# Optimization experiments

Hardware: AMD Instinct MI355X
Metric: run time of the kernel (lower is better)

The kernel has to match this reference:

```python
import jax, jax.numpy as jnp
import numpy as np

B, S, E, H = 2, 2048, 1024, 16
D = E // H  # head_dim = 64


def setup_inputs() -> dict:
    key = jax.random.key(0)
    ks = jax.random.split(key, 12)
    s = 1.0 / np.sqrt(E)
    return {
        "queries": jax.random.normal(ks[0], (B, S, E), jnp.float32),
        "keys": jax.random.normal(ks[1], (B, S, E), jnp.float32),
        "values": jax.random.normal(ks[2], (B, S, E), jnp.float32),
        "mask": jnp.zeros((B, 1, S, S), jnp.float32),
        "Wq": jax.random.normal(ks[3], (E, E), jnp.float32) * s,
        "bq": jnp.zeros((E,), jnp.float32),
        "Wk": jax.random.normal(ks[4], (E, E), jnp.float32) * s,
        "bk": jnp.zeros((E,), jnp.float32),
        "Wv": jax.random.normal(ks[5], (E, E), jnp.float32) * s,
        "bv": jnp.zeros((E,), jnp.float32),
        "Wo": jax.random.normal(ks[6], (E, E), jnp.float32) * s,
        "bo": jnp.zeros((E,), jnp.float32),
    }


def reference(queries, keys, values, mask, Wq, bq, Wk, bk, Wv, bv, Wo, bo):
    # QKV projections, then split heads: [B,S,E] -> [B,H,S,D]
    def split_heads(x):
        return x.reshape(B, S, H, D).transpose(0, 2, 1, 3)

    Q = split_heads(queries @ Wq + bq)
    K = split_heads(keys @ Wk + bk)
    V = split_heads(values @ Wv + bv)
    scale = jnp.sqrt(jnp.asarray(D, jnp.float32))
    # [B,H,S,S] attention scores
    scores = jnp.einsum("bhqd,bhkd->bhqk", Q, K) / scale
    scores = scores + mask * -10000.0
    weights = jax.nn.softmax(scores, axis=-1)
    # [B,H,S,D] -> [B,S,E]
    out = jnp.einsum("bhqk,bhkd->bhqd", weights, V)
    out = out.transpose(0, 2, 1, 3).reshape(B, S, E)
    return out @ Wo + bo
```

## Files before the change

kernel.cpp:

```cpp
#include <hip/hip_runtime.h>
#include <hip/hip_bf16.h>
#include <stdint.h>

#define B_ 2
#define S_ 2048
#define E_ 1024
#define H_ 16
#define D_ 64
#define LOG2E 1.4426950408889634f

typedef unsigned short ubf;
typedef __attribute__((ext_vector_type(8))) short bh8;
typedef __attribute__((ext_vector_type(4))) float fx4;
typedef __attribute__((ext_vector_type(16))) float fx16;

__device__ __forceinline__ ubf f2bf(float f) {
  unsigned u = __float_as_uint(f);
  unsigned r = (u + 0x7fffu + ((u >> 16) & 1u)) >> 16;
  return (ubf)r;
}

__device__ __forceinline__ unsigned cvtpk(float lo, float hi2) {
  unsigned r;
  asm("v_cvt_pk_bf16_f32 %0, %1, %2" : "=v"(r) : "v"(lo), "v"(hi2));
  return r;
}

__device__ __forceinline__ void pl32swap(unsigned& a, unsigned& b) {
  asm("v_permlane32_swap_b32 %0, %1" : "+v"(a), "+v"(b));
}

__device__ __forceinline__ void gl_lds16(const void* g, void* l) {
  __builtin_amdgcn_global_load_lds(
      (const __attribute__((address_space(1))) void*)g,
      (__attribute__((address_space(3))) void*)l, 16, 0, 0);
}

__global__ void prep(const float* __restrict__ q, const float* __restrict__ k,
                     const float* __restrict__ v, const float* __restrict__ mask,
                     ubf* __restrict__ dst0, int* __restrict__ flagarr) {
  const int z = blockIdx.z;
  const int tid = threadIdx.x;
  const int stride = gridDim.x * blockDim.x;
  if (z == 3) {
    int any = 0;
    const int n4m = (B_ * S_ * S_) / 4;
    for (int j = blockIdx.x * blockDim.x + tid; j < n4m; j += stride) {
      float4 x = ((const float4*)mask)[j];
      any |= (x.x != 0.f) | (x.y != 0.f) | (x.z != 0.f) | (x.w != 0.f);
    }
    int wany = __any(any != 0) ? 1 : 0;
    if ((tid & 63) == 0) flagarr[blockIdx.x * 4 + (tid >> 6)] = wany;
    return;
  }
  const float* src = (z == 0) ? q : (z == 1) ? k : v;
  ubf* dst = dst0 + (size_t)z * (B_ * S_ * E_);
  const int n4 = (B_ * S_ * E_) / 4;
  for (int j = blockIdx.x * blockDim.x + tid; j < n4; j += stride) {
    float4 x = ((const float4*)src)[j];
    ushort4 o;
    o.x = f2bf(x.x); o.y = f2bf(x.y); o.z = f2bf(x.z); o.w = f2bf(x.w);
    ((ushort4*)dst)[j] = o;
  }
}

__global__ void wtrans4(const float* __restrict__ Wq, const float* __restrict__ Wk,
                        const float* __restrict__ Wv, const float* __restrict__ Wo,
                        ubf* __restrict__ Wt0) {
  __shared__ float t[32][33];
  int z = blockIdx.z;
  const float* W = (z == 0) ? Wq : (z == 1) ? Wk : (z == 2) ? Wv : Wo;
  ubf* Wt = Wt0 + (size_t)z * (E_ * E_);
  int kb = blockIdx.x, nb = blockIdx.y;
  int c = threadIdx.x & 31, r0 = threadIdx.x >> 5;
#pragma unroll
  for (int rr = 0; rr < 32; rr += 8)
    t[r0 + rr][c] = W[(size_t)(kb * 32 + r0 + rr) * E_ + nb * 32 + c];
  __syncthreads();
#pragma unroll
  for (int rr = 0; rr < 32; rr += 8)
    Wt[(size_t)(nb * 32 + r0 + rr) * E_ + kb * 32 + c] = f2bf(t[c][r0 + rr]);
}

__global__ void __launch_bounds__(256, 6)
gemm_qkv(const ubf* __restrict__ X, const ubf* __restrict__ Wt,
         const float* __restrict__ bq, const float* __restrict__ bk,
         const float* __restrict__ bv, ubf* __restrict__ Out) {
  constexpr int K = 1024;
  __shared__ ubf Asm[2][128 * 32];
  __shared__ ubf Bsm[2][64 * 32];
  const int z = blockIdx.z;
  const ubf* A  = (z == 2) ? (Wt + 2u * 1048576u) : (X + (size_t)z * 4194304u);
  const ubf* Bt = (z == 2) ? (X + 2u * 4194304u) : (Wt + (size_t)z * 1048576u);
  const float* bias = (z == 0) ? bq : (z == 1) ? bk : bv;
  ubf* Cout = Out + (size_t)z * 4194304u;

  const int bx0 = blockIdx.x;
  const int swz = (bx0 & 7) * 64 + (bx0 >> 3);
  int bm, bn;
  if (z == 2) {
    bm = (swz >> 3) & 7;
    bn = ((swz >> 6) << 3) | (swz & 7);
  } else {
    bm = swz >> 4;
    bn = swz & 15;
  }

  const int tid = threadIdx.x;
  const int lane = tid & 63, w = tid >> 6;
  const int wm = w >> 1, wn = w & 1;
  const int g = lane >> 4, c15 = lane & 15;

  const fx4 FZ = {0.f, 0.f, 0.f, 0.f};
  fx4 acc[4][2];
#pragma unroll
  for (int m = 0; m < 4; m++)
#pragma unroll
    for (int n = 0; n < 2; n++) acc[m][n] = FZ;

  auto stage = [&](int buf, int k0) {
#pragma unroll
    for (int i = 0; i < 2; i++) {
      int s = i * 256 + tid;
      int row = s >> 2, cc = s & 3;
      int sc = cc ^ ((row >> 1) & 3);
      gl_lds16(A + (size_t)(bm * 128 + row) * K + k0 + sc * 8,
               (char*)&Asm[buf][0] + (i * 256 + (tid & 192)) * 16);
    }
    {
      int row = tid >> 2, cc = tid & 3;
      int sc = cc ^ ((row >> 1) & 3);
      gl_lds16(Bt + (size_t)(bn * 64 + row) * K + k0 + sc * 8,
               (char*)&Bsm[buf][0] + (tid & 192) * 16);
    }
  };

  stage(0, 0);
  for (int t = 0; t < K / 32; t++) {
    int cur = t & 1;
    if (t + 1 < K / 32) {
      stage(cur ^ 1, (t + 1) * 32);
      asm volatile("s_waitcnt vmcnt(3)" ::: "memory");
    } else {
      asm volatile("s_waitcnt vmcnt(0)" ::: "memory");
    }
    __builtin_amdgcn_s_barrier();
    bh8 a[4], b[2];
#pragma unroll
    for (int m = 0; m < 4; m++) {
      int row = wm * 64 + m * 16 + c15;
      int ch = g ^ ((row >> 1) & 3);
      a[m] = *(const bh8*)((const char*)&Asm[cur][0] + row * 64 + ch * 16);
    }
#pragma unroll
    for (int n = 0; n < 2; n++) {
      int row = wn * 32 + n * 16 + c15;
      int ch = g ^ ((row >> 1) & 3);
      b[n] = *(const bh8*)((const char*)&Bsm[cur][0] + row * 64 + ch * 16);
    }
    __builtin_amdgcn_s_setprio(1);
#pragma unroll
    for (int m = 0; m < 4; m++)
#pragma unroll
      for (int n = 0; n < 2; n++)
        acc[m][n] = __builtin_amdgcn_mfma_f32_16x16x32_bf16(a[m], b[n], acc[m][n], 0, 0, 0);
    __builtin_amdgcn_s_setprio(0);
    __builtin_amdgcn_s_barrier();
  }

#pragma unroll
  for (int m = 0; m < 4; m++) {
    int rbase = bm * 128 + wm * 64 + m * 16 + g * 4;
#pragma unroll
    for (int n = 0; n < 2; n++) {
      int col = bn * 64 + wn * 32 + n * 16 + c15;
#pragma unroll
      for (int r = 0; r < 4; r++) {
        int mrow = rbase + r;
        float val = acc[m][n][r];
        if (z <= 1) {
          val = val + bias[col];
          if (z == 0) val *= 0.125f * LOG2E;
          int bb = mrow >> 11, ss = mrow & 2047, hh = col >> 6, dd = col & 63;
          Cout[((size_t)(bb * H_ + hh) * S_ + ss) * D_ + dd] = f2bf(val);
        } else {
          val = val + bias[mrow];
          int bb = col >> 11, ss = col & 2047, hh = mrow >> 6, dd = mrow & 63;
          Cout[((size_t)(bb * H_ + hh) * D_ + dd) * S_ + ss] = f2bf(val);
        }
      }
    }
  }
}

__global__ void __launch_bounds__(256, 4)
gemm_out(const ubf* __restrict__ A, const ubf* __restrict__ Bt,
         const float* __restrict__ bias, float* __restrict__ Cout, int N) {
  constexpr int K = 1024;
  __shared__ ubf Asm[2][64 * 32];
  __shared__ ubf Bsm[2][64 * 32];
  const int tid = threadIdx.x;
  const int lane = tid & 63, w = tid >> 6;
  const int wm = w >> 1, wn = w & 1;
  const int bid = blockIdx.x;
  const int swz = (bid & 7) * 128 + (bid >> 3);
  const int bm = swz >> 4, bn = swz & 15;
  const int g = lane >> 4, c15 = lane & 15;

  const fx4 FZ = {0.f, 0.f, 0.f, 0.f};
  fx4 acc[2][2];
#pragma unroll
  for (int m = 0; m < 2; m++)
#pragma unroll
    for (int n = 0; n < 2; n++) acc[m][n] = FZ;

  auto stage = [&](int buf, int k0) {
    int row = tid >> 2, cc = tid & 3;
    int sc = cc ^ ((row >> 1) & 3);
    gl_lds16(A + (size_t)(bm * 64 + row) * K + k0 + sc * 8,
             (char*)&Asm[buf][0] + (tid & 192) * 16);
    gl_lds16(Bt + (size_t)(bn * 64 + row) * K + k0 + sc * 8,
             (char*)&Bsm[buf][0] + (tid & 192) * 16);
  };

  stage(0, 0);
  for (int t = 0; t < K / 32; t++) {
    int cur = t & 1;
    if (t + 1 < K / 32) {
      stage(cur ^ 1, (t + 1) * 32);
      asm volatile("s_waitcnt vmcnt(2)" ::: "memory");
    } else {
      asm volatile("s_waitcnt vmcnt(0)" ::: "memory");
    }
    __builtin_amdgcn_s_barrier();
    bh8 a[2], b[2];
#pragma unroll
    for (int m = 0; m < 2; m++) {
      int row = wm * 32 + m * 16 + c15;
      int ch = g ^ ((row >> 1) & 3);
      a[m] = *(const bh8*)((const char*)&Asm[cur][0] + row * 64 + ch * 16);
    }
#pragma unroll
    for (int n = 0; n < 2; n++) {
      int row = wn * 32 + n * 16 + c15;
      int ch = g ^ ((row >> 1) & 3);
      b[n] = *(const bh8*)((const char*)&Bsm[cur][0] + row * 64 + ch * 16);
    }
    __builtin_amdgcn_s_setprio(1);
#pragma unroll
    for (int m = 0; m < 2; m++)
#pragma unroll
      for (int n = 0; n < 2; n++)
        acc[m][n] = __builtin_amdgcn_mfma_f32_16x16x32_bf16(a[m], b[n], acc[m][n], 0, 0, 0);
    __builtin_amdgcn_s_setprio(0);
    __builtin_amdgcn_s_barrier();
  }

#pragma unroll
  for (int m = 0; m < 2; m++) {
    int rbase = bm * 64 + wm * 32 + m * 16 + g * 4;
#pragma unroll
    for (int n = 0; n < 2; n++) {
      int col = bn * 64 + wn * 32 + n * 16 + c15;
#pragma unroll
      for (int r = 0; r < 4; r++)
        Cout[(size_t)(rbase + r) * N + col] = acc[m][n][r] + bias[col];
    }
  }
}

#define ROWQ(r) (((r) & 3) + 8 * ((r) >> 2) + 4 * hi)

__global__ void __launch_bounds__(512, 2)
flash_fast(const ubf* __restrict__ Q, const ubf* __restrict__ Kh,
           const ubf* __restrict__ Vt, ubf* __restrict__ AO) {
  __shared__ char lds[65536];
  const int tid = threadIdx.x, lane = tid & 63, w = tid >> 6;
  const int grp = w >> 2, wq = w & 3, tin = tid & 255;
  const int l31 = lane & 31, hi = lane >> 5;
  const int bh = blockIdx.x;
  const int qb = blockIdx.y;
  const int b = bh >> 4, h = bh & 15;
  const int k00 = grp * (S_ / 2);
  constexpr int NT = (S_ / 2) / 64;

  const ubf* Qrow = Q + ((size_t)bh * S_ + qb * 128 + wq * 32 + l31) * D_;
  bh8 q4[4];
#pragma unroll
  for (int kf = 0; kf < 4; kf++) q4[kf] = *(const bh8*)(Qrow + kf * 16 + hi * 8);

  fx16 acc0, acc1, ZF;
#pragma unroll
  for (int i = 0; i < 16; i++) { acc0[i] = 0.f; acc1[i] = 0.f; ZF[i] = 0.f; }
  float2 lr2 = make_float2(0.f, 0.f);

  const ubf* Kg = Kh + (size_t)bh * S_ * D_;
  const ubf* Vg = Vt + (size_t)bh * D_ * S_;
  char* Kbase = lds + grp * 32768;

  auto stage = [&](int buf, int k0) {
    char* Kb = Kbase + buf * 16384;
#pragma unroll
    for (int i = 0; i < 2; i++) {
      int s = i * 256 + tin;
      int row = s >> 3, cc = s & 7;
      int sw = cc ^ (row & 7);
      gl_lds16(Kg + (size_t)(k0 + row) * D_ + sw * 8,
               Kb + (i * 256 + (tin & 192)) * 16);
      gl_lds16(Vg + (size_t)row * S_ + k0 + sw * 8,
               Kb + 8192 + (i * 256 + (tin & 192)) * 16);
    }
  };

  stage(0, k00);

  for (int t = 0; t < NT; t++) {
    int cur = t & 1;
    if (t + 1 < NT) {
      stage(cur ^ 1, k00 + (t + 1) * 64);
      asm volatile("s_waitcnt vmcnt(4)" ::: "memory");
    } else {
      asm volatile("s_waitcnt vmcnt(0)" ::: "memory");
    }
    __builtin_amdgcn_s_barrier();
    const char* Kc = Kbase + cur * 16384;
    const char* Vc = Kc + 8192;

#pragma unroll
    for (int h2 = 0; h2 < 2; h2++) {
      fx16 sc;
      __builtin_amdgcn_s_setprio(1);
      {
        int ch = hi ^ (l31 & 7);
        bh8 ak = *(const bh8*)(Kc + (h2 * 32 + l31) * 128 + ch * 16);
        sc = __builtin_amdgcn_mfma_f32_32x32x16_bf16(ak, q4[0], ZF, 0, 0, 0);
      }
#pragma unroll
      for (int kf = 1; kf < 4; kf++) {
        int ch = (2 * kf + hi) ^ (l31 & 7);
        bh8 ak = *(const bh8*)(Kc + (h2 * 32 + l31) * 128 + ch * 16);
        sc = __builtin_amdgcn_mfma_f32_32x32x16_bf16(ak, q4[kf], sc, 0, 0, 0);
      }
      __builtin_amdgcn_s_setprio(0);

#pragma unroll
      for (int i = 0; i < 8; i++) {
        float p0 = __builtin_amdgcn_exp2f(sc[2 * i]);
        float p1 = __builtin_amdgcn_exp2f(sc[2 * i + 1]);
        sc[2 * i] = p0; sc[2 * i + 1] = p1;
        lr2.x += p0; lr2.y += p1;
      }

      unsigned pk[8];
#pragma unroll
      for (int i = 0; i < 8; i++) pk[i] = cvtpk(sc[2 * i], sc[2 * i + 1]);
      pl32swap(pk[0], pk[2]); pl32swap(pk[1], pk[3]);
      pl32swap(pk[4], pk[6]); pl32swap(pk[5], pk[7]);

      __builtin_amdgcn_s_setprio(1);
#pragma unroll
      for (int kk = 0; kk < 2; kk++) {
        int KF = 2 * h2 + kk;
        int ch = (2 * KF + hi) ^ (l31 & 7);
        bh8 bv0 = *(const bh8*)(Vc + l31 * 128 + ch * 16);
        bh8 bv1 = *(const bh8*)(Vc + (32 + l31) * 128 + ch * 16);
        unsigned wa[4] = {pk[4 * kk], pk[4 * kk + 1], pk[4 * kk + 2], pk[4 * kk + 3]};
        bh8 pa = *(bh8*)wa;
        acc0 = __builtin_amdgcn_mfma_f32_32x32x16_bf16(pa, bv0, acc0, 0, 0, 0);
        acc1 = __builtin_amdgcn_mfma_f32_32x32x16_bf16(pa, bv1, acc1, 0, 0, 0);
      }
      __builtin_amdgcn_s_setprio(0);
    }
    __builtin_amdgcn_s_barrier();
  }

  float lrun = lr2.x + lr2.y;
  float lsum = lrun + __shfl_xor(lrun, 32);
  float* shacc = (float*)lds;
  float* shml  = (float*)(lds + 34816);
  if (grp == 1) {
    float* p = shacc + (size_t)(wq * 64 + lane) * 34;
#pragma unroll
    for (int r = 0; r < 16; r++) { p[r] = acc0[r]; p[16 + r] = acc1[r]; }
    if (hi == 0) shml[wq * 32 + l31] = lsum;
  }
  __syncthreads();
  if (grp == 0) {
    const float* p = shacc + (size_t)(wq * 64 + lane) * 34;
#pragma unroll
    for (int r = 0; r < 16; r++) {
      int q2 = ROWQ(r);
      float l0 = __shfl(lsum, q2);
      float inv = 1.0f / (l0 + shml[wq * 32 + q2]);
      size_t base = ((size_t)(b * S_ + qb * 128 + wq * 32 + q2)) * E_ + h * 64;
      AO[base + l31] = f2bf((acc0[r] + p[r]) * inv);
      AO[base + 32 + l31] = f2bf((acc1[r] + p[16 + r]) * inv);
    }
  }
}

#define PV_STEP(KF, W0, W1, W2, W3)                                             \
    {                                                                           \
      unsigned wa[4] = {W0, W1, W2, W3};                                        \
      bh8 pa = *(bh8*)wa;                                                       \
      int ch = (2 * (KF) + hi) ^ (l31 & 7);                                     \
      bh8 bv0 = *(const bh8*)(Vc + l31 * 128 + ch * 16);                        \
      acc0 = __builtin_amdgcn_mfma_f32_32x32x16_bf16(pa, bv0, acc0, 0, 0, 0);   \
      bh8 bv1 = *(const bh8*)(Vc + (32 + l31) * 128 + ch * 16);                 \
      acc1 = __builtin_amdgcn_mfma_f32_32x32x16_bf16(pa, bv1, acc1, 0, 0, 0);   \
    }

__global__ void __launch_bounds__(256, 4)
flash_masked(const ubf* __restrict__ Q, const ubf* __restrict__ Kh,
             const ubf* __restrict__ Vt, const float* __restrict__ mask,
             const int* __restrict__ flagarr, ubf* __restrict__ AO) {
  __shared__ int anyf;
  if (threadIdx.x == 0) anyf = 0;
  __syncthreads();
  {
    int a = 0;
#pragma unroll
    for (int i = 0; i < 8; i++) a |= flagarr[threadIdx.x + i * 256];
    if (a) anyf = 1;
  }
  __syncthreads();
  if (anyf == 0) return;

  __shared__ ubf Ksm[2][64 * 64];
  __shared__ ubf Vsm[2][64 * 64];
  const int tid = threadIdx.x, lane = tid & 63, w = tid >> 6;
  const int l31 = lane & 31, hi = lane >> 5;
  const int bh = blockIdx.x;
  const int qb = blockIdx.y;
  const int b = bh >> 4, h = bh & 15;
  const int qg = qb * 128 + w * 32 + l31;
  constexpr int NT = S_ / 64;

  const ubf* Qrow = Q + ((size_t)bh * S_ + qg) * D_;
  bh8 q4[4];
#pragma unroll
  for (int kf = 0; kf < 4; kf++) q4[kf] = *(const bh8*)(Qrow + kf * 16 + hi * 8);

  fx16 acc0, acc1;
#pragma unroll
  for (int i = 0; i < 16; i++) { acc0[i] = 0.f; acc1[i] = 0.f; }
  float mrun = -3.0e38f, lrun = 0.f;

  const ubf* Kg = Kh + (size_t)bh * S_ * D_;
  const ubf* Vg = Vt + (size_t)bh * D_ * S_;

  auto stage = [&](int buf, int k0) {
#pragma unroll
    for (int i = 0; i < 2; i++) {
      int s = i * 256 + tid;
      int row = s >> 3, cc = s & 7;
      int sw = cc ^ (row & 7);
      gl_lds16(Kg + (size_t)(k0 + row) * D_ + sw * 8,
               (char*)&Ksm[buf][0] + (i * 256 + (tid & 192)) * 16);
      gl_lds16(Vg + (size_t)row * S_ + k0 + sw * 8,
               (char*)&Vsm[buf][0] + (i * 256 + (tid & 192)) * 16);
    }
  };

  stage(0, 0);
  __syncthreads();

  for (int t = 0; t < NT; t++) {
    int cur = t & 1;
    if (t + 1 < NT) stage(cur ^ 1, (t + 1) * 64);
    const char* Kc = (const char*)&Ksm[cur][0];
    const char* Vc = (const char*)&Vsm[cur][0];

#pragma unroll
    for (int h2 = 0; h2 < 2; h2++) {
      fx16 sc;
#pragma unroll
      for (int i = 0; i < 16; i++) sc[i] = 0.f;
#pragma unroll
      for (int kf = 0; kf < 4; kf++) {
        int ch = (2 * kf + hi) ^ (l31 & 7);
        bh8 ak = *(const bh8*)(Kc + (h2 * 32 + l31) * 128 + ch * 16);
        sc = __builtin_amdgcn_mfma_f32_32x32x16_bf16(ak, q4[kf], sc, 0, 0, 0);
      }
      const float* mq = mask + ((size_t)(b * S_ + qg)) * S_ + t * 64 + h2 * 32;
#pragma unroll
      for (int r = 0; r < 16; r++)
        sc[r] += mq[ROWQ(r)] * (-14426.950408889634f);

      float pm = sc[0];
#pragma unroll
      for (int r = 1; r < 16; r++) pm = fmaxf(pm, sc[r]);
      pm = fmaxf(pm, __shfl_xor(pm, 32));
      if (__any(pm - mrun > 11.5415603f)) {
        float mnew = fmaxf(mrun, pm);
        float al = exp2f(mrun - mnew);
        lrun *= al;
#pragma unroll
        for (int r = 0; r < 16; r++) {
          float alr = __shfl(al, ROWQ(r));
          acc0[r] *= alr;
          acc1[r] *= alr;
        }
        mrun = mnew;
      }
      float rsv[4] = {0.f, 0.f, 0.f, 0.f};
#pragma unroll
      for (int i = 0; i < 16; i++) {
        float p = exp2f(sc[i] - mrun);
        sc[i] = p;
        rsv[i & 3] += p;
      }
      lrun += (rsv[0] + rsv[1]) + (rsv[2] + rsv[3]);

      unsigned pk[8];
#pragma unroll
      for (int i = 0; i < 8; i++) pk[i] = cvtpk(sc[2 * i], sc[2 * i + 1]);
      pl32swap(pk[0], pk[2]); pl32swap(pk[1], pk[3]);
      pl32swap(pk[4], pk[6]); pl32swap(pk[5], pk[7]);

      PV_STEP(2 * h2,     pk[0], pk[1], pk[2], pk[3])
      PV_STEP(2 * h2 + 1, pk[4], pk[5], pk[6], pk[7])
    }
    __syncthreads();
  }

  float ltot = lrun + __shfl_xor(lrun, 32);
#pragma unroll
  for (int r = 0; r < 16; r++) {
    int q2 = ROWQ(r);
    float linv = 1.0f / __shfl(ltot, q2);
    size_t base = ((size_t)(b * S_ + qb * 128 + w * 32 + q2)) * E_ + h * 64;
    AO[base + l31] = f2bf(acc0[r] * linv);
    AO[base + 32 + l31] = f2bf(acc1[r] * linv);
  }
}

extern "C" void kernel_launch(void* const* d_in, const int* in_sizes, int n_in,
                              void* d_out, int out_size, void* d_ws, size_t ws_size,
                              hipStream_t stream) {
  (void)in_sizes; (void)n_in; (void)out_size; (void)ws_size;
  const float* q  = (const float*)d_in[0];
  const float* k  = (const float*)d_in[1];
  const float* v  = (const float*)d_in[2];
  const float* mask = (const float*)d_in[3];
  const float* Wq = (const float*)d_in[4];
  const float* bq = (const float*)d_in[5];
  const float* Wk = (const float*)d_in[6];
  const float* bk = (const float*)d_in[7];
  const float* Wv = (const float*)d_in[8];
  const float* bv = (const float*)d_in[9];
  const float* Wo = (const float*)d_in[10];
  const float* bo = (const float*)d_in[11];

  char* ws = (char*)d_ws;
  ubf* X    = (ubf*)(ws);
  ubf* Wt0  = (ubf*)(ws + 25165824);
  ubf* Qh   = (ubf*)(ws + 33554432);
  ubf* Kh   = (ubf*)(ws + 41943040);
  ubf* Vt   = (ubf*)(ws + 50331648);
  ubf* AO   = (ubf*)(ws + 58720256);
  int* flagarr = (int*)(ws + 67108864);

  ubf* Wot = Wt0 + 3145728;

  prep<<<dim3(512, 1, 4), 256, 0, stream>>>(q, k, v, mask, X, flagarr);
  wtrans4<<<dim3(32, 32, 4), 256, 0, stream>>>(Wq, Wk, Wv, Wo, Wt0);

  gemm_qkv<<<dim3(512, 1, 3), 256, 0, stream>>>(X, Wt0, bq, bk, bv, Qh);

  flash_fast<<<dim3(32, 16), 512, 0, stream>>>(Qh, Kh, Vt, AO);
  flash_masked<<<dim3(32, 16), 256, 0, stream>>>(Qh, Kh, Vt, mask, flagarr, AO);

  gemm_out<<<dim3(1024), 256, 0, stream>>>(AO, Wot, bo, (float*)d_out, 1024);
}
```

Measured before the change: 134.2 us.

## Fuse fp32-to-bf16 activation conversion into QKV projection GEMM loads

The prep kernel no longer converts q/k/v to a bf16 workspace. Instead, the QKV GEMM loads fp32 activations into registers, converts them with packed bf16 conversion, and writes them to swizzled LDS, while weights still go through direct global-to-LDS loads. This removes a full write and re-read of 24 MB of bf16 activations and one pass of the prep kernel. In exchange the GEMM reads fp32 data (twice the bytes per tile, and each tile is re-read across the N blocks), adds register pressure, and drops the occupancy hint from launch bounds. The new pipeline also waits on vmcnt(0) each iteration, which weakens load/compute overlap.

```diff
diff --git a/kernel.cpp b/kernel.cpp
--- a/kernel.cpp
+++ b/kernel.cpp
@@ -36,32 +36,17 @@
       (__attribute__((address_space(3))) void*)l, 16, 0, 0);
 }
 
-__global__ void prep(const float* __restrict__ q, const float* __restrict__ k,
-                     const float* __restrict__ v, const float* __restrict__ mask,
-                     ubf* __restrict__ dst0, int* __restrict__ flagarr) {
-  const int z = blockIdx.z;
+__global__ void maskscan(const float* __restrict__ mask, int* __restrict__ flagarr) {
   const int tid = threadIdx.x;
   const int stride = gridDim.x * blockDim.x;
-  if (z == 3) {
-    int any = 0;
-    const int n4m = (B_ * S_ * S_) / 4;
-    for (int j = blockIdx.x * blockDim.x + tid; j < n4m; j += stride) {
-      float4 x = ((const float4*)mask)[j];
-      any |= (x.x != 0.f) | (x.y != 0.f) | (x.z != 0.f) | (x.w != 0.f);
-    }
-    int wany = __any(any != 0) ? 1 : 0;
-    if ((tid & 63) == 0) flagarr[blockIdx.x * 4 + (tid >> 6)] = wany;
-    return;
-  }
-  const float* src = (z == 0) ? q : (z == 1) ? k : v;
-  ubf* dst = dst0 + (size_t)z * (B_ * S_ * E_);
-  const int n4 = (B_ * S_ * E_) / 4;
-  for (int j = blockIdx.x * blockDim.x + tid; j < n4; j += stride) {
-    float4 x = ((const float4*)src)[j];
-    ushort4 o;
-    o.x = f2bf(x.x); o.y = f2bf(x.y); o.z = f2bf(x.z); o.w = f2bf(x.w);
-    ((ushort4*)dst)[j] = o;
-  }
+  int any = 0;
+  const int n4m = (B_ * S_ * S_) / 4;
+  for (int j = blockIdx.x * blockDim.x + tid; j < n4m; j += stride) {
+    float4 x = ((const float4*)mask)[j];
+    any |= (x.x != 0.f) | (x.y != 0.f) | (x.z != 0.f) | (x.w != 0.f);
+  }
+  int wany = __any(any != 0) ? 1 : 0;
+  if ((tid & 63) == 0) flagarr[blockIdx.x * 4 + (tid >> 6)] = wany;
 }
 
 __global__ void wtrans4(const float* __restrict__ Wq, const float* __restrict__ Wk,
@@ -82,16 +67,18 @@
     Wt[(size_t)(nb * 32 + r0 + rr) * E_ + kb * 32 + c] = f2bf(t[c][r0 + rr]);
 }
 
-__global__ void __launch_bounds__(256, 6)
-gemm_qkv(const ubf* __restrict__ X, const ubf* __restrict__ Wt,
+__global__ void __launch_bounds__(256)
+gemm_qkv(const float* __restrict__ q, const float* __restrict__ k,
+         const float* __restrict__ v, const ubf* __restrict__ Wt,
          const float* __restrict__ bq, const float* __restrict__ bk,
          const float* __restrict__ bv, ubf* __restrict__ Out) {
   constexpr int K = 1024;
+  constexpr int NTT = K / 32;
   __shared__ ubf Asm[2][128 * 32];
   __shared__ ubf Bsm[2][64 * 32];
   const int z = blockIdx.z;
-  const ubf* A  = (z == 2) ? (Wt + 2u * 1048576u) : (X + (size_t)z * 4194304u);
-  const ubf* Bt = (z == 2) ? (X + 2u * 4194304u) : (Wt + (size_t)z * 1048576u);
+  const float* Fsrc = (z == 0) ? q : (z == 1) ? k : v;
+  const ubf* Wsrc = (z == 2) ? (Wt + 2u * 1048576u) : (Wt + (size_t)z * 1048576u);
   const float* bias = (z == 0) ? bq : (z == 1) ? bk : bv;
   ubf* Cout = Out + (size_t)z * 4194304u;
 
@@ -110,6 +97,7 @@
   const int lane = tid & 63, w = tid >> 6;
   const int wm = w >> 1, wn = w & 1;
   const int g = lane >> 4, c15 = lane & 15;
+  const int rr = tid >> 2, qq = tid & 3;
 
   const fx4 FZ = {0.f, 0.f, 0.f, 0.f};
   fx4 acc[4][2];
@@ -118,33 +106,90 @@
 #pragma unroll
     for (int n = 0; n < 2; n++) acc[m][n] = FZ;
 
-  auto stage = [&](int buf, int k0) {
-#pragma unroll
-    for (int i = 0; i < 2; i++) {
-      int s = i * 256 + tid;
-      int row = s >> 2, cc = s & 3;
-      int sc = cc ^ ((row >> 1) & 3);
-      gl_lds16(A + (size_t)(bm * 128 + row) * K + k0 + sc * 8,
-               (char*)&Asm[buf][0] + (i * 256 + (tid & 192)) * 16);
-    }
-    {
+  float4 fa0, fa1, fa2, fa3;
+
+  auto issue = [&](int k0) {
+    if (z < 2) {
+      const float* s0 = Fsrc + (size_t)(bm * 128 + rr) * K + k0 + qq * 8;
+      fa0 = *(const float4*)s0;
+      fa1 = *(const float4*)(s0 + 4);
+      const float* s1 = s0 + (size_t)64 * K;
+      fa2 = *(const float4*)s1;
+      fa3 = *(const float4*)(s1 + 4);
+      {
+        int row = tid >> 2, cc = tid & 3;
+        int sc = cc ^ ((row >> 1) & 3);
+        gl_lds16(Wsrc + (size_t)(bn * 64 + row) * K + k0 + sc * 8, nullptr);
+      }
+    } else {
+      const float* s0 = Fsrc + (size_t)(bn * 64 + rr) * K + k0 + qq * 8;
+      fa0 = *(const float4*)s0;
+      fa1 = *(const float4*)(s0 + 4);
+#pragma unroll
+      for (int i = 0; i < 2; i++) {
+        int s = i * 256 + tid;
+        int row = s >> 2, cc = s & 3;
+        int sc = cc ^ ((row >> 1) & 3);
+        gl_lds16(Wsrc + (size_t)(bm * 128 + row) * K + k0 + sc * 8, nullptr);
+      }
+    }
+  };
+
+  (void)issue;
+
+  auto issue_to = [&](int buf, int k0) {
+    if (z < 2) {
+      const float* s0 = Fsrc + (size_t)(bm * 128 + rr) * K + k0 + qq * 8;
+      fa0 = *(const float4*)s0;
+      fa1 = *(const float4*)(s0 + 4);
+      const float* s1 = s0 + (size_t)64 * K;
+      fa2 = *(const float4*)s1;
+      fa3 = *(const float4*)(s1 + 4);
       int row = tid >> 2, cc = tid & 3;
       int sc = cc ^ ((row >> 1) & 3);
-      gl_lds16(Bt + (size_t)(bn * 64 + row) * K + k0 + sc * 8,
+      gl_lds16(Wsrc + (size_t)(bn * 64 + row) * K + k0 + sc * 8,
                (char*)&Bsm[buf][0] + (tid & 192) * 16);
+    } else {
+      const float* s0 = Fsrc + (size_t)(bn * 64 + rr) * K + k0 + qq * 8;
+      fa0 = *(const float4*)s0;
+      fa1 = *(const float4*)(s0 + 4);
+#pragma unroll
+      for (int i = 0; i < 2; i++) {
+        int s = i * 256 + tid;
+        int row = s >> 2, cc = s & 3;
+        int sc = cc ^ ((row >> 1) & 3);
+        gl_lds16(Wsrc + (size_t)(bm * 128 + row) * K + k0 + sc * 8,
+                 (char*)&Asm[buf][0] + (i * 256 + (tid & 192)) * 16);
+      }
     }
   };
 
-  stage(0, 0);
-  for (int t = 0; t < K / 32; t++) {
+  auto write_cvt = [&](int buf) {
+    int slot = qq ^ ((rr >> 1) & 3);
+    if (z < 2) {
+      unsigned u0[4] = {cvtpk(fa0.x, fa0.y), cvtpk(fa0.z, fa0.w),
+                        cvtpk(fa1.x, fa1.y), cvtpk(fa1.z, fa1.w)};
+      *(bh8*)((char*)&Asm[buf][0] + rr * 64 + slot * 16) = *(bh8*)u0;
+      unsigned u1[4] = {cvtpk(fa2.x, fa2.y), cvtpk(fa2.z, fa2.w),
+                        cvtpk(fa3.x, fa3.y), cvtpk(fa3.z, fa3.w)};
+      *(bh8*)((char*)&Asm[buf][0] + (rr + 64) * 64 + slot * 16) = *(bh8*)u1;
+    } else {
+      unsigned u0[4] = {cvtpk(fa0.x, fa0.y), cvtpk(fa0.z, fa0.w),
+                        cvtpk(fa1.x, fa1.y), cvtpk(fa1.z, fa1.w)};
+      *(bh8*)((char*)&Bsm[buf][0] + rr * 64 + slot * 16) = *(bh8*)u0;
+    }
+  };
+
+  issue_to(0, 0);
+  asm volatile("s_waitcnt vmcnt(0)" ::: "memory");
+  write_cvt(0);
+  asm volatile("s_waitcnt lgkmcnt(0)" ::: "memory");
+  __builtin_amdgcn_s_barrier();
+
+  for (int t = 0; t < NTT; t++) {
     int cur = t & 1;
-    if (t + 1 < K / 32) {
-      stage(cur ^ 1, (t + 1) * 32);
-      asm volatile("s_waitcnt vmcnt(3)" ::: "memory");
-    } else {
-      asm volatile("s_waitcnt vmcnt(0)" ::: "memory");
-    }
-    __builtin_amdgcn_s_barrier();
+    if (t + 1 < NTT) issue_to(cur ^ 1, (t + 1) * 32);
+
     bh8 a[4], b[2];
 #pragma unroll
     for (int m = 0; m < 4; m++) {
@@ -165,7 +210,13 @@
       for (int n = 0; n < 2; n++)
         acc[m][n] = __builtin_amdgcn_mfma_f32_16x16x32_bf16(a[m], b[n], acc[m][n], 0, 0, 0);
     __builtin_amdgcn_s_setprio(0);
-    __builtin_amdgcn_s_barrier();
+
+    if (t + 1 < NTT) {
+      asm volatile("s_waitcnt vmcnt(0)" ::: "memory");
+      write_cvt(cur ^ 1);
+      asm volatile("s_waitcnt lgkmcnt(0)" ::: "memory");
+      __builtin_amdgcn_s_barrier();
+    }
   }
 
 #pragma unroll
@@ -553,7 +604,6 @@
   const float* bo = (const float*)d_in[11];
 
   char* ws = (char*)d_ws;
-  ubf* X    = (ubf*)(ws);
   ubf* Wt0  = (ubf*)(ws + 25165824);
   ubf* Qh   = (ubf*)(ws + 33554432);
   ubf* Kh   = (ubf*)(ws + 41943040);
@@ -563,10 +613,10 @@
 
   ubf* Wot = Wt0 + 3145728;
 
-  prep<<<dim3(512, 1, 4), 256, 0, stream>>>(q, k, v, mask, X, flagarr);
+  maskscan<<<512, 256, 0, stream>>>(mask, flagarr);
   wtrans4<<<dim3(32, 32, 4), 256, 0, stream>>>(Wq, Wk, Wv, Wo, Wt0);
 
-  gemm_qkv<<<dim3(512, 1, 3), 256, 0, stream>>>(X, Wt0, bq, bk, bv, Qh);
+  gemm_qkv<<<dim3(512, 1, 3), 256, 0, stream>>>(q, k, v, Wt0, bq, bk, bv, Qh);
 
   flash_fast<<<dim3(32, 16), 512, 0, stream>>>(Qh, Kh, Vt, AO);
   flash_masked<<<dim3(32, 16), 256, 0, stream>>>(Qh, Kh, Vt, mask, flagarr, AO);
```

Result: slower. 137.8 us (+2.7%).

## Load GEMM operands directly from global into registers, dropping LDS staging

Applied to the files above, without the earlier changes.

The QKV and output projection GEMMs no longer stage tiles through double-buffered LDS with direct-to-LDS loads and barriers. Each wave now reads its MFMA operands straight from global memory into registers, and the loop is unrolled by four so loads can run ahead. This removes the LDS traffic and the workgroup barriers, and occupancy hints are adjusted to match. The cost is that waves sharing a tile each fetch the same data from global memory, so redundant loads lean on the L2 cache, and each row access reads only a 64-byte chunk.

```diff
diff --git a/kernel.cpp b/kernel.cpp
--- a/kernel.cpp
+++ b/kernel.cpp
@@ -82,13 +82,11 @@
     Wt[(size_t)(nb * 32 + r0 + rr) * E_ + kb * 32 + c] = f2bf(t[c][r0 + rr]);
 }
 
-__global__ void __launch_bounds__(256, 6)
+__global__ void __launch_bounds__(256, 5)
 gemm_qkv(const ubf* __restrict__ X, const ubf* __restrict__ Wt,
          const float* __restrict__ bq, const float* __restrict__ bk,
          const float* __restrict__ bv, ubf* __restrict__ Out) {
   constexpr int K = 1024;
-  __shared__ ubf Asm[2][128 * 32];
-  __shared__ ubf Bsm[2][64 * 32];
   const int z = blockIdx.z;
   const ubf* A  = (z == 2) ? (Wt + 2u * 1048576u) : (X + (size_t)z * 4194304u);
   const ubf* Bt = (z == 2) ? (X + 2u * 4194304u) : (Wt + (size_t)z * 1048576u);
@@ -118,46 +116,19 @@
 #pragma unroll
     for (int n = 0; n < 2; n++) acc[m][n] = FZ;
 
-  auto stage = [&](int buf, int k0) {
-#pragma unroll
-    for (int i = 0; i < 2; i++) {
-      int s = i * 256 + tid;
-      int row = s >> 2, cc = s & 3;
-      int sc = cc ^ ((row >> 1) & 3);
-      gl_lds16(A + (size_t)(bm * 128 + row) * K + k0 + sc * 8,
-               (char*)&Asm[buf][0] + (i * 256 + (tid & 192)) * 16);
-    }
-    {
-      int row = tid >> 2, cc = tid & 3;
-      int sc = cc ^ ((row >> 1) & 3);
-      gl_lds16(Bt + (size_t)(bn * 64 + row) * K + k0 + sc * 8,
-               (char*)&Bsm[buf][0] + (tid & 192) * 16);
-    }
-  };
-
-  stage(0, 0);
+  const ubf* Ap = A + (size_t)(bm * 128 + wm * 64 + c15) * K + g * 8;
+  const ubf* Bp = Bt + (size_t)(bn * 64 + wn * 32 + c15) * K + g * 8;
+
+#pragma unroll 4
   for (int t = 0; t < K / 32; t++) {
-    int cur = t & 1;
-    if (t + 1 < K / 32) {
-      stage(cur ^ 1, (t + 1) * 32);
-      asm volatile("s_waitcnt vmcnt(3)" ::: "memory");
-    } else {
-      asm volatile("s_waitcnt vmcnt(0)" ::: "memory");
-    }
-    __builtin_amdgcn_s_barrier();
+    const int ko = t * 32;
     bh8 a[4], b[2];
 #pragma unroll
-    for (int m = 0; m < 4; m++) {
-      int row = wm * 64 + m * 16 + c15;
-      int ch = g ^ ((row >> 1) & 3);
-      a[m] = *(const bh8*)((const char*)&Asm[cur][0] + row * 64 + ch * 16);
-    }
-#pragma unroll
-    for (int n = 0; n < 2; n++) {
-      int row = wn * 32 + n * 16 + c15;
-      int ch = g ^ ((row >> 1) & 3);
-      b[n] = *(const bh8*)((const char*)&Bsm[cur][0] + row * 64 + ch * 16);
-    }
+    for (int m = 0; m < 4; m++)
+      a[m] = *(const bh8*)(Ap + (size_t)(m * 16) * K + ko);
+#pragma unroll
+    for (int n = 0; n < 2; n++)
+      b[n] = *(const bh8*)(Bp + (size_t)(n * 16) * K + ko);
     __builtin_amdgcn_s_setprio(1);
 #pragma unroll
     for (int m = 0; m < 4; m++)
@@ -165,7 +136,6 @@
       for (int n = 0; n < 2; n++)
         acc[m][n] = __builtin_amdgcn_mfma_f32_16x16x32_bf16(a[m], b[n], acc[m][n], 0, 0, 0);
     __builtin_amdgcn_s_setprio(0);
-    __builtin_amdgcn_s_barrier();
   }
 
 #pragma unroll
@@ -193,12 +163,10 @@
   }
 }
 
-__global__ void __launch_bounds__(256, 4)
+__global__ void __launch_bounds__(256, 6)
 gemm_out(const ubf* __restrict__ A, const ubf* __restrict__ Bt,
          const float* __restrict__ bias, float* __restrict__ Cout, int N) {
   constexpr int K = 1024;
-  __shared__ ubf Asm[2][64 * 32];
-  __shared__ ubf Bsm[2][64 * 32];
   const int tid = threadIdx.x;
   const int lane = tid & 63, w = tid >> 6;
   const int wm = w >> 1, wn = w & 1;
@@ -214,38 +182,19 @@
 #pragma unroll
     for (int n = 0; n < 2; n++) acc[m][n] = FZ;
 
-  auto stage = [&](int buf, int k0) {
-    int row = tid >> 2, cc = tid & 3;
-    int sc = cc ^ ((row >> 1) & 3);
-    gl_lds16(A + (size_t)(bm * 64 + row) * K + k0 + sc * 8,
-             (char*)&Asm[buf][0] + (tid & 192) * 16);
-    gl_lds16(Bt + (size_t)(bn * 64 + row) * K + k0 + sc * 8,
-             (char*)&Bsm[buf][0] + (tid & 192) * 16);
-  };
-
-  stage(0, 0);
+  const ubf* Ap = A + (size_t)(bm * 64 + wm * 32 + c15) * K + g * 8;
+  const ubf* Bp = Bt + (size_t)(bn * 64 + wn * 32 + c15) * K + g * 8;
+
+#pragma unroll 4
   for (int t = 0; t < K / 32; t++) {
-    int cur = t & 1;
-    if (t + 1 < K / 32) {
-      stage(cur ^ 1, (t + 1) * 32);
-      asm volatile("s_waitcnt vmcnt(2)" ::: "memory");
-    } else {
-      asm volatile("s_waitcnt vmcnt(0)" ::: "memory");
-    }
-    __builtin_amdgcn_s_barrier();
+    const int ko = t * 32;
     bh8 a[2], b[2];
 #pragma unroll
-    for (int m = 0; m < 2; m++) {
-      int row = wm * 32 + m * 16 + c15;
-      int ch = g ^ ((row >> 1) & 3);
-      a[m] = *(const bh8*)((const char*)&Asm[cur][0] + row * 64 + ch * 16);
-    }
-#pragma unroll
-    for (int n = 0; n < 2; n++) {
-      int row = wn * 32 + n * 16 + c15;
-      int ch = g ^ ((row >> 1) & 3);
-      b[n] = *(const bh8*)((const char*)&Bsm[cur][0] + row * 64 + ch * 16);
-    }
+    for (int m = 0; m < 2; m++)
+      a[m] = *(const bh8*)(Ap + (size_t)(m * 16) * K + ko);
+#pragma unroll
+    for (int n = 0; n < 2; n++)
+      b[n] = *(const bh8*)(Bp + (size_t)(n * 16) * K + ko);
     __builtin_amdgcn_s_setprio(1);
 #pragma unroll
     for (int m = 0; m < 2; m++)
@@ -253,7 +202,6 @@
       for (int n = 0; n < 2; n++)
         acc[m][n] = __builtin_amdgcn_mfma_f32_16x16x32_bf16(a[m], b[n], acc[m][n], 0, 0, 0);
     __builtin_amdgcn_s_setprio(0);
-    __builtin_amdgcn_s_barrier();
   }
 
 #pragma unroll
```

Result: slower. 260.3 us (+93.9%).
